# Kernel optimization log

Hardware: AMD Instinct MI355X
Metric: run time of the kernel (lower is better)

## Reference

```python
import jax, jax.numpy as jnp
import numpy as np

EPS = 1e-05
N = 8192


def setup_inputs() -> dict:
    key = jax.random.key(0)
    k1, k2 = jax.random.split(key)
    params = jax.random.normal(k1, (3,), dtype=jnp.float32) * 0.1
    # sparse-ish symmetric 0/1 adjacency, float32 like the torch buffer
    a = (jax.random.uniform(k2, (N, N)) < 0.005).astype(jnp.float32)
    graph = jnp.maximum(a, a.T)
    return {"params": params, "graph": graph}


def reference(params, graph):
    alpha, beta, sigma = params[0], params[1], params[2]
    n = graph.shape[0]
    # p == 0 => sum_degrees(v) is just the degree (row sum) of v
    deg = jnp.sum(graph, axis=1)                       # [n]
    s = alpha * deg[:, None] + beta * deg[None, :] + sigma   # [n, n]
    p = 1.0 / (1.0 + jnp.exp(s))                        # logistic prob
    ll = jnp.where(graph == 1.0,
                   jnp.log(p + EPS),
                   jnp.log(1.0 - p + EPS))
    # loop runs over i <= j: upper triangle including diagonal
    upper = jnp.triu(jnp.ones((n, n), dtype=bool))
    likelihood = jnp.sum(jnp.where(upper, ll, 0.0))
    return -likelihood
```

## Files before the change

### kernel.cpp

```cpp
#include <hip/hip_runtime.h>

#define N 8192
#define EPS 1e-5f
#define LOG2E 1.4426950408889634f
#define LN2d  0.6931471805599453

#define TR 64
#define TC 256
#define NBJ 32
#define NBI 128
#define RPW 16
#define CAPW 512
#define SEG_W 4096
#define NTILES 2112
#define NSEG (NTILES * 4)
#define NDENSE 4096
#define NFB 1024

static const size_t OFF_ACC = 0;
static const size_t OFF_OVF = 4096;
static const size_t OFF_DEG = 4224;
static const size_t OFF_CNT = OFF_DEG + (size_t)N * 4;
static const size_t OFF_EDG = OFF_CNT + (size_t)NSEG * 4;
static const size_t WS_NEED = OFF_EDG + (size_t)NSEG * SEG_W * 4;

__device__ __forceinline__ unsigned mbcnt64(unsigned long long m) {
    return __builtin_amdgcn_mbcnt_hi((unsigned)(m >> 32),
           __builtin_amdgcn_mbcnt_lo((unsigned)m, 0u));
}

__global__ void k_init(float* __restrict__ deg, double* __restrict__ accv,
                       unsigned* __restrict__ ovf, const int segmode) {
    const int t = blockIdx.x * 256 + threadIdx.x;
    if (t < 512) accv[t] = 0.0;
    if (t == 513) *ovf = segmode ? 0u : 1u;
    if (t < N) deg[t] = 0.f;
}

__global__ __launch_bounds__(256) void k_pass1(const float* __restrict__ g,
        float* __restrict__ deg, unsigned* __restrict__ cnt,
        unsigned* __restrict__ edges, const int segmode) {
    const int bj = (int)blockIdx.x & (NBJ - 1);
    const int bi = (int)blockIdx.x >> 5;
    if (bi > 4 * bj + 3) return;
    const int r0 = bi * TR, c0 = bj * TC;
    const int wave = threadIdx.x >> 6, lane = threadIdx.x & 63;
    const int aid = 2 * bj * (bj + 1) + bi;

    __shared__ float    scol[TC];
    __shared__ unsigned buf[4][CAPW];
    scol[threadIdx.x] = 0.f;
    __syncthreads();

    const int c = c0 + lane * 4;
    const int rbase = r0 + wave * RPW;
    const float* __restrict__ gp = g + (size_t)rbase * N + c;
    unsigned* __restrict__ myseg = edges + ((size_t)aid * 4 + wave) * SEG_W;
    unsigned wc = 0, wflushed = 0;
    float ca0 = 0.f, ca1 = 0.f, ca2 = 0.f, ca3 = 0.f;

#define EMIT(BB, PRED, OFFv) \
    if (BB) { if (segmode && (PRED)) buf[wave][wc + mbcnt64(BB)] = etag | (OFFv); \
        const unsigned p_ = __popcll(BB); wc += p_; rsum += p_; }

#define FLUSHCHK \
    if (segmode && wc > (unsigned)(CAPW - 256)) { \
        for (unsigned t_ = lane; t_ < wc; t_ += 64) myseg[wflushed + t_] = buf[wave][t_]; \
        wflushed += wc; wc = 0; }

    if (r0 + TR <= c0) {
        #pragma unroll 4
        for (int k = 0; k < RPW; ++k) {
            const float4 v = *reinterpret_cast<const float4*>(gp + (size_t)k * N);
            FLUSHCHK
            ca0 += v.x; ca1 += v.y; ca2 += v.z; ca3 += v.w;
            const unsigned long long b0 = __ballot(v.x != 0.f);
            const unsigned long long b1 = __ballot(v.y != 0.f);
            const unsigned long long b2 = __ballot(v.z != 0.f);
            const unsigned long long b3 = __ballot(v.w != 0.f);
            if (b0 | b1 | b2 | b3) {
                const int gr = rbase + k;
                const unsigned etag = ((unsigned)gr << 16) | (unsigned)c;
                unsigned rsum = 0;
                EMIT(b0, v.x != 0.f, 0u)
                EMIT(b1, v.y != 0.f, 1u)
                EMIT(b2, v.z != 0.f, 2u)
                EMIT(b3, v.w != 0.f, 3u)
                if (lane == 0) atomicAdd(&deg[gr], (float)rsum);
            }
        }
    } else {
        for (int k = 0; k < RPW; ++k) {
            const int gr = rbase + k;
            const float4 v = *reinterpret_cast<const float4*>(gp + (size_t)k * N);
            FLUSHCHK
            const bool a0 = (v.x != 0.f) && (c + 0 >= gr);
            const bool a1 = (v.y != 0.f) && (c + 1 >= gr);
            const bool a2 = (v.z != 0.f) && (c + 2 >= gr);
            const bool a3 = (v.w != 0.f) && (c + 3 >= gr);
            ca0 += (c + 0 > gr) ? v.x : 0.f;
            ca1 += (c + 1 > gr) ? v.y : 0.f;
            ca2 += (c + 2 > gr) ? v.z : 0.f;
            ca3 += (c + 3 > gr) ? v.w : 0.f;
            const unsigned long long b0 = __ballot(a0);
            const unsigned long long b1 = __ballot(a1);
            const unsigned long long b2 = __ballot(a2);
            const unsigned long long b3 = __ballot(a3);
            if (b0 | b1 | b2 | b3) {
                const unsigned etag = ((unsigned)gr << 16) | (unsigned)c;
                unsigned rsum = 0;
                EMIT(b0, a0, 0u)
                EMIT(b1, a1, 1u)
                EMIT(b2, a2, 2u)
                EMIT(b3, a3, 3u)
                if (lane == 0) atomicAdd(&deg[gr], (float)rsum);
            }
        }
    }
#undef EMIT
#undef FLUSHCHK

    if (segmode) {
        for (unsigned t = lane; t < wc; t += 64) myseg[wflushed + t] = buf[wave][t];
        if (lane == 0) cnt[aid * 4 + wave] = wflushed + wc;
    }
    if (ca0 != 0.f) atomicAdd(&scol[lane * 4 + 0], ca0);
    if (ca1 != 0.f) atomicAdd(&scol[lane * 4 + 1], ca1);
    if (ca2 != 0.f) atomicAdd(&scol[lane * 4 + 2], ca2);
    if (ca3 != 0.f) atomicAdd(&scol[lane * 4 + 3], ca3);
    __syncthreads();
    const float sv = scol[threadIdx.x];
    if (sv != 0.f) atomicAdd(&deg[c0 + threadIdx.x], sv);
}

__global__ __launch_bounds__(256) void k_ll(const float* __restrict__ g,
        const float* __restrict__ deg, const float* __restrict__ params,
        const unsigned* __restrict__ cnt, const unsigned* __restrict__ edges,
        const unsigned* __restrict__ ovf, double* __restrict__ accv) {
    const int b = blockIdx.x;
    const unsigned o = *ovf;
    const float alpha = params[0], beta = params[1], sigma = params[2];
    double dlocal = 0.0;

    if (b < NDENSE) {
        if (o) return;
        const int r1 = b, r2 = N - 1 - b;
        const float b2 = beta * LOG2E;
        const float base1 = fmaf(alpha, deg[r1], sigma) * LOG2E;
        const float base2 = fmaf(alpha, deg[r2], sigma) * LOG2E;
        float l0 = 0.f, l1 = 0.f, l2 = 0.f, l3 = 0.f;

#define DELEM(J, ACC, BASE) { \
        const float s2_ = fmaf(b2, deg[J], BASE); \
        const float e_  = __builtin_amdgcn_exp2f(s2_); \
        const float p_  = __builtin_amdgcn_rcpf(1.f + e_); \
        ACC += __builtin_amdgcn_logf(1.00001f - p_); }

        int j = r1 + (int)threadIdx.x;
        for (; j + 768 < N; j += 1024) {
            DELEM(j,       l0, base1)
            DELEM(j + 256, l1, base1)
            DELEM(j + 512, l2, base1)
            DELEM(j + 768, l3, base1)
        }
        for (; j < N; j += 256) DELEM(j, l0, base1)

        j = r2 + (int)threadIdx.x;
        for (; j + 768 < N; j += 1024) {
            DELEM(j,       l0, base2)
            DELEM(j + 256, l1, base2)
            DELEM(j + 512, l2, base2)
            DELEM(j + 768, l3, base2)
        }
        for (; j < N; j += 256) DELEM(j, l1, base2)
#undef DELEM
        dlocal = (double)((l0 + l1) + (l2 + l3)) * LN2d;
    } else if (b < NDENSE + NTILES) {
        if (o) return;
        const int aid = b - NDENSE;
        float local = 0.f;
        for (int w = 0; w < 4; ++w) {
            const unsigned n = cnt[aid * 4 + w];
            const unsigned* __restrict__ seg = edges + ((size_t)aid * 4 + w) * SEG_W;
            for (unsigned t = threadIdx.x; t < n; t += 256) {
                const unsigned e = seg[t];
                const float di = deg[e >> 16];
                const float dj = deg[e & 0xffffu];
                const float s = fmaf(alpha, di, fmaf(beta, dj, sigma));
                const float p = __fdividef(1.f, 1.f + __expf(s));
                local += __logf(p + EPS) - __logf(1.f - p + EPS);
            }
        }
        dlocal = (double)local;
    } else {
        if (!o) return;
        const int rb = b - NDENSE - NTILES;
        for (int q = 0; q < 8; ++q) {
            const int i = rb * 8 + q;
            const float base = fmaf(alpha, deg[i], sigma);
            float rl = 0.f;
            for (int j = i + (int)threadIdx.x; j < N; j += 256) {
                const float s = fmaf(beta, deg[j], base);
                const float p = __fdividef(1.f, 1.f + __expf(s));
                const float gv = g[(size_t)i * N + j];
                rl += (gv != 0.f) ? __logf(p + EPS) : __logf(1.f - p + EPS);
            }
            dlocal += (double)rl;
        }
    }

    #pragma unroll
    for (int off = 32; off; off >>= 1) dlocal += __shfl_xor(dlocal, off);
    __shared__ double wsum[4];
    const int wv = threadIdx.x >> 6, ln = threadIdx.x & 63;
    if (ln == 0) wsum[wv] = dlocal;
    __syncthreads();
    if (threadIdx.x == 0) {
        const double t = (wsum[0] + wsum[1]) + (wsum[2] + wsum[3]);
        if (t != 0.0) atomicAdd(&accv[(b & 63) * 8], t);
    }
}

__global__ void k_final(const double* __restrict__ accv, float* __restrict__ out) {
    double v = accv[threadIdx.x * 8];
    #pragma unroll
    for (int off = 32; off; off >>= 1) v += __shfl_xor(v, off);
    if (threadIdx.x == 0) out[0] = (float)(-v);
}

extern "C" void kernel_launch(void* const* d_in, const int* in_sizes, int n_in,
                              void* d_out, int out_size, void* d_ws, size_t ws_size,
                              hipStream_t stream) {
    const float* params = (const float*)d_in[0];
    const float* graph  = (const float*)d_in[1];
    float* out = (float*)d_out;

    char* ws = (char*)d_ws;
    double*   accv  = (double*)(ws + OFF_ACC);
    unsigned* ovf   = (unsigned*)(ws + OFF_OVF);
    float*    deg   = (float*)(ws + OFF_DEG);
    unsigned* cnt   = (unsigned*)(ws + OFF_CNT);
    unsigned* edges = (unsigned*)(ws + OFF_EDG);
    const int segmode = (ws_size >= WS_NEED) ? 1 : 0;

    k_init<<<32, 256, 0, stream>>>(deg, accv, ovf, segmode);
    k_pass1<<<NBI * NBJ, 256, 0, stream>>>(graph, deg, cnt, edges, segmode);
    k_ll<<<NDENSE + NTILES + NFB, 256, 0, stream>>>(graph, deg, params, cnt, edges, ovf, accv);
    k_final<<<1, 64, 0, stream>>>(accv, out);
}
```

Baseline: 59.70 us.

## Shrink pass-1 tiles to 16 rows, drop flush logic, replace init kernel with memset

Reduces the row tile from 64 to 16 rows so pass 1 launches four times as many blocks, each wave loading its four rows up front with no loop and no mid-tile buffer flush. Edge segments shrink accordingly, and the likelihood kernel's edge blocks now each walk 16 segments so the edge-block count stays the same. The init kernel is replaced by a hipMemsetAsync, and the overflow flag becomes a host-side argument, which also trims the fallback blocks from the grid in segment mode. The goal is more parallelism and memory-level overlap in the graph read. The cost is more block launches and more deg atomics per column tile, plus a risk of overflowing the 1024-entry per-wave buffer on dense rows.

Measured after the change: 98.22 us. +64.5%, slower.

```diff
diff --git a/kernel.cpp b/kernel.cpp
--- a/kernel.cpp
+++ b/kernel.cpp
@@ -5,21 +5,21 @@
 #define LOG2E 1.4426950408889634f
 #define LN2d  0.6931471805599453
 
-#define TR 64
+#define TR 16
 #define TC 256
 #define NBJ 32
-#define NBI 128
-#define RPW 16
-#define CAPW 512
-#define SEG_W 4096
-#define NTILES 2112
+#define NBI 512
+#define RPW 4
+#define CAPW 1024
+#define SEG_W 1024
+#define NTILES 8448
 #define NSEG (NTILES * 4)
 #define NDENSE 4096
+#define NEDGE 2112
 #define NFB 1024
 
 static const size_t OFF_ACC = 0;
-static const size_t OFF_OVF = 4096;
-static const size_t OFF_DEG = 4224;
+static const size_t OFF_DEG = 4096;
 static const size_t OFF_CNT = OFF_DEG + (size_t)N * 4;
 static const size_t OFF_EDG = OFF_CNT + (size_t)NSEG * 4;
 static const size_t WS_NEED = OFF_EDG + (size_t)NSEG * SEG_W * 4;
@@ -27,14 +27,6 @@
 __device__ __forceinline__ unsigned mbcnt64(unsigned long long m) {
     return __builtin_amdgcn_mbcnt_hi((unsigned)(m >> 32),
            __builtin_amdgcn_mbcnt_lo((unsigned)m, 0u));
-}
-
-__global__ void k_init(float* __restrict__ deg, double* __restrict__ accv,
-                       unsigned* __restrict__ ovf, const int segmode) {
-    const int t = blockIdx.x * 256 + threadIdx.x;
-    if (t < 512) accv[t] = 0.0;
-    if (t == 513) *ovf = segmode ? 0u : 1u;
-    if (t < N) deg[t] = 0.f;
 }
 
 __global__ __launch_bounds__(256) void k_pass1(const float* __restrict__ g,
@@ -42,10 +34,10 @@
         unsigned* __restrict__ edges, const int segmode) {
     const int bj = (int)blockIdx.x & (NBJ - 1);
     const int bi = (int)blockIdx.x >> 5;
-    if (bi > 4 * bj + 3) return;
+    if (bi > 16 * bj + 15) return;
     const int r0 = bi * TR, c0 = bj * TC;
     const int wave = threadIdx.x >> 6, lane = threadIdx.x & 63;
-    const int aid = 2 * bj * (bj + 1) + bi;
+    const int aid = 8 * bj * (bj + 1) + bi;
 
     __shared__ float    scol[TC];
     __shared__ unsigned buf[4][CAPW];
@@ -56,73 +48,69 @@
     const int rbase = r0 + wave * RPW;
     const float* __restrict__ gp = g + (size_t)rbase * N + c;
     unsigned* __restrict__ myseg = edges + ((size_t)aid * 4 + wave) * SEG_W;
-    unsigned wc = 0, wflushed = 0;
+    unsigned wc = 0;
     float ca0 = 0.f, ca1 = 0.f, ca2 = 0.f, ca3 = 0.f;
 
 #define EMIT(BB, PRED, OFFv) \
     if (BB) { if (segmode && (PRED)) buf[wave][wc + mbcnt64(BB)] = etag | (OFFv); \
         const unsigned p_ = __popcll(BB); wc += p_; rsum += p_; }
 
-#define FLUSHCHK \
-    if (segmode && wc > (unsigned)(CAPW - 256)) { \
-        for (unsigned t_ = lane; t_ < wc; t_ += 64) myseg[wflushed + t_] = buf[wave][t_]; \
-        wflushed += wc; wc = 0; }
-
-    if (r0 + TR <= c0) {
-        #pragma unroll 4
-        for (int k = 0; k < RPW; ++k) {
-            const float4 v = *reinterpret_cast<const float4*>(gp + (size_t)k * N);
-            FLUSHCHK
-            ca0 += v.x; ca1 += v.y; ca2 += v.z; ca3 += v.w;
-            const unsigned long long b0 = __ballot(v.x != 0.f);
-            const unsigned long long b1 = __ballot(v.y != 0.f);
-            const unsigned long long b2 = __ballot(v.z != 0.f);
-            const unsigned long long b3 = __ballot(v.w != 0.f);
-            if (b0 | b1 | b2 | b3) {
-                const int gr = rbase + k;
-                const unsigned etag = ((unsigned)gr << 16) | (unsigned)c;
-                unsigned rsum = 0;
-                EMIT(b0, v.x != 0.f, 0u)
-                EMIT(b1, v.y != 0.f, 1u)
-                EMIT(b2, v.z != 0.f, 2u)
-                EMIT(b3, v.w != 0.f, 3u)
-                if (lane == 0) atomicAdd(&deg[gr], (float)rsum);
-            }
-        }
+    const float4 v0 = *reinterpret_cast<const float4*>(gp);
+    const float4 v1 = *reinterpret_cast<const float4*>(gp + (size_t)N);
+    const float4 v2 = *reinterpret_cast<const float4*>(gp + 2 * (size_t)N);
+    const float4 v3 = *reinterpret_cast<const float4*>(gp + 3 * (size_t)N);
+
+    if (bi < 16 * bj) {
+#define PROCA(V, K) { \
+        ca0 += V.x; ca1 += V.y; ca2 += V.z; ca3 += V.w; \
+        const unsigned long long b0 = __ballot(V.x != 0.f); \
+        const unsigned long long b1 = __ballot(V.y != 0.f); \
+        const unsigned long long b2 = __ballot(V.z != 0.f); \
+        const unsigned long long b3 = __ballot(V.w != 0.f); \
+        if (b0 | b1 | b2 | b3) { \
+            const int gr = rbase + (K); \
+            const unsigned etag = ((unsigned)gr << 16) | (unsigned)c; \
+            unsigned rsum = 0; \
+            EMIT(b0, V.x != 0.f, 0u) \
+            EMIT(b1, V.y != 0.f, 1u) \
+            EMIT(b2, V.z != 0.f, 2u) \
+            EMIT(b3, V.w != 0.f, 3u) \
+            if (lane == 0) atomicAdd(&deg[gr], (float)rsum); \
+        } }
+        PROCA(v0, 0) PROCA(v1, 1) PROCA(v2, 2) PROCA(v3, 3)
+#undef PROCA
     } else {
-        for (int k = 0; k < RPW; ++k) {
-            const int gr = rbase + k;
-            const float4 v = *reinterpret_cast<const float4*>(gp + (size_t)k * N);
-            FLUSHCHK
-            const bool a0 = (v.x != 0.f) && (c + 0 >= gr);
-            const bool a1 = (v.y != 0.f) && (c + 1 >= gr);
-            const bool a2 = (v.z != 0.f) && (c + 2 >= gr);
-            const bool a3 = (v.w != 0.f) && (c + 3 >= gr);
-            ca0 += (c + 0 > gr) ? v.x : 0.f;
-            ca1 += (c + 1 > gr) ? v.y : 0.f;
-            ca2 += (c + 2 > gr) ? v.z : 0.f;
-            ca3 += (c + 3 > gr) ? v.w : 0.f;
-            const unsigned long long b0 = __ballot(a0);
-            const unsigned long long b1 = __ballot(a1);
-            const unsigned long long b2 = __ballot(a2);
-            const unsigned long long b3 = __ballot(a3);
-            if (b0 | b1 | b2 | b3) {
-                const unsigned etag = ((unsigned)gr << 16) | (unsigned)c;
-                unsigned rsum = 0;
-                EMIT(b0, a0, 0u)
-                EMIT(b1, a1, 1u)
-                EMIT(b2, a2, 2u)
-                EMIT(b3, a3, 3u)
-                if (lane == 0) atomicAdd(&deg[gr], (float)rsum);
-            }
-        }
+#define PROCD(V, K) { \
+        const int gr = rbase + (K); \
+        const bool a0 = (V.x != 0.f) && (c + 0 >= gr); \
+        const bool a1 = (V.y != 0.f) && (c + 1 >= gr); \
+        const bool a2 = (V.z != 0.f) && (c + 2 >= gr); \
+        const bool a3 = (V.w != 0.f) && (c + 3 >= gr); \
+        ca0 += (c + 0 > gr) ? V.x : 0.f; \
+        ca1 += (c + 1 > gr) ? V.y : 0.f; \
+        ca2 += (c + 2 > gr) ? V.z : 0.f; \
+        ca3 += (c + 3 > gr) ? V.w : 0.f; \
+        const unsigned long long b0 = __ballot(a0); \
+        const unsigned long long b1 = __ballot(a1); \
+        const unsigned long long b2 = __ballot(a2); \
+        const unsigned long long b3 = __ballot(a3); \
+        if (b0 | b1 | b2 | b3) { \
+            const unsigned etag = ((unsigned)gr << 16) | (unsigned)c; \
+            unsigned rsum = 0; \
+            EMIT(b0, a0, 0u) \
+            EMIT(b1, a1, 1u) \
+            EMIT(b2, a2, 2u) \
+            EMIT(b3, a3, 3u) \
+            if (lane == 0) atomicAdd(&deg[gr], (float)rsum); \
+        } }
+        PROCD(v0, 0) PROCD(v1, 1) PROCD(v2, 2) PROCD(v3, 3)
+#undef PROCD
     }
 #undef EMIT
-#undef FLUSHCHK
 
     if (segmode) {
-        for (unsigned t = lane; t < wc; t += 64) myseg[wflushed + t] = buf[wave][t];
-        if (lane == 0) cnt[aid * 4 + wave] = wflushed + wc;
+        for (unsigned t = lane; t < wc; t += 64) myseg[t] = buf[wave][t];
+        if (lane == 0) cnt[aid * 4 + wave] = wc;
     }
     if (ca0 != 0.f) atomicAdd(&scol[lane * 4 + 0], ca0);
     if (ca1 != 0.f) atomicAdd(&scol[lane * 4 + 1], ca1);
@@ -136,14 +124,12 @@
 __global__ __launch_bounds__(256) void k_ll(const float* __restrict__ g,
         const float* __restrict__ deg, const float* __restrict__ params,
         const unsigned* __restrict__ cnt, const unsigned* __restrict__ edges,
-        const unsigned* __restrict__ ovf, double* __restrict__ accv) {
+        double* __restrict__ accv, const int segmode) {
     const int b = blockIdx.x;
-    const unsigned o = *ovf;
     const float alpha = params[0], beta = params[1], sigma = params[2];
     double dlocal = 0.0;
 
     if (b < NDENSE) {
-        if (o) return;
         const int r1 = b, r2 = N - 1 - b;
         const float b2 = beta * LOG2E;
         const float base1 = fmaf(alpha, deg[r1], sigma) * LOG2E;
@@ -175,26 +161,27 @@
         for (; j < N; j += 256) DELEM(j, l1, base2)
 #undef DELEM
         dlocal = (double)((l0 + l1) + (l2 + l3)) * LN2d;
-    } else if (b < NDENSE + NTILES) {
-        if (o) return;
-        const int aid = b - NDENSE;
+        if (segmode == 0) dlocal = 0.0;
+    } else if (b < NDENSE + NEDGE) {
+        if (!segmode) return;
+        const int t16 = b - NDENSE;
         float local = 0.f;
-        for (int w = 0; w < 4; ++w) {
-            const unsigned n = cnt[aid * 4 + w];
-            const unsigned* __restrict__ seg = edges + ((size_t)aid * 4 + w) * SEG_W;
+        for (int s = t16 * 16; s < t16 * 16 + 16; ++s) {
+            const unsigned n = cnt[s];
+            const unsigned* __restrict__ seg = edges + (size_t)s * SEG_W;
             for (unsigned t = threadIdx.x; t < n; t += 256) {
                 const unsigned e = seg[t];
                 const float di = deg[e >> 16];
                 const float dj = deg[e & 0xffffu];
-                const float s = fmaf(alpha, di, fmaf(beta, dj, sigma));
-                const float p = __fdividef(1.f, 1.f + __expf(s));
+                const float sc = fmaf(alpha, di, fmaf(beta, dj, sigma));
+                const float p = __fdividef(1.f, 1.f + __expf(sc));
                 local += __logf(p + EPS) - __logf(1.f - p + EPS);
             }
         }
         dlocal = (double)local;
     } else {
-        if (!o) return;
-        const int rb = b - NDENSE - NTILES;
+        if (segmode) return;
+        const int rb = b - NDENSE - NEDGE;
         for (int q = 0; q < 8; ++q) {
             const int i = rb * 8 + q;
             const float base = fmaf(alpha, deg[i], sigma);
@@ -237,14 +224,14 @@
 
     char* ws = (char*)d_ws;
     double*   accv  = (double*)(ws + OFF_ACC);
-    unsigned* ovf   = (unsigned*)(ws + OFF_OVF);
     float*    deg   = (float*)(ws + OFF_DEG);
     unsigned* cnt   = (unsigned*)(ws + OFF_CNT);
     unsigned* edges = (unsigned*)(ws + OFF_EDG);
     const int segmode = (ws_size >= WS_NEED) ? 1 : 0;
 
-    k_init<<<32, 256, 0, stream>>>(deg, accv, ovf, segmode);
+    hipMemsetAsync(ws, 0, OFF_DEG + (size_t)N * 4, stream);
     k_pass1<<<NBI * NBJ, 256, 0, stream>>>(graph, deg, cnt, edges, segmode);
-    k_ll<<<NDENSE + NTILES + NFB, 256, 0, stream>>>(graph, deg, params, cnt, edges, ovf, accv);
+    const int llgrid = segmode ? (NDENSE + NEDGE) : (NDENSE + NEDGE + NFB);
+    k_ll<<<llgrid, 256, 0, stream>>>(graph, deg, params, cnt, edges, accv, segmode);
     k_final<<<1, 64, 0, stream>>>(accv, out);
 }
```
